# Optimization experiments

Measured on AMD Instinct MI355X. Metric: run time of the kernel, lower is better.

The kernel has to match this reference:

```python
import jax, jax.numpy as jnp
import numpy as np

# ---- static configuration (matches init_kwargs) ----
D_MODEL = 512
N_HEAD = 16
HEAD_DIM = D_MODEL // N_HEAD
SCALE = HEAD_DIM ** -0.5
SIZE = (64, 64)
WINDOW = (8, 8)
SHIFT = (4, 4)
WS = WINDOW[0] * WINDOW[1]          # tokens per window = 64
NW = (SIZE[0] // WINDOW[0]) * (SIZE[1] // WINDOW[1])  # windows per sample = 64


def _rel_pos_index(window):
    w0, w1 = window
    coords = np.stack(np.meshgrid(np.arange(w0), np.arange(w1), indexing='ij')).reshape(2, -1)
    rel = (coords[:, :, None] - coords[:, None, :]).transpose(1, 2, 0)  # [ws, ws, 2]
    rel[:, :, 0] += w0 - 1
    rel[:, :, 1] += w1 - 1
    rel[:, :, 0] *= 2 * w1 - 1
    return rel.sum(-1)  # [ws, ws] in [0, (2w0-1)(2w1-1))


def _shift_mask(size, window, shift):
    # Swin-style attention mask for shifted windows: 1.0 where tokens belong
    # to different cyclic-shift regions, else 0.0. Shape [nw, ws, ws].
    H, W = size
    w0, w1 = window
    s0, s1 = shift
    img = np.zeros((H, W))
    cnt = 0
    h_slices = (slice(0, -w0), slice(-w0, -s0), slice(-s0, None)) if s0 > 0 else (slice(None),)
    w_slices = (slice(0, -w1), slice(-w1, -s1), slice(-s1, None)) if s1 > 0 else (slice(None),)
    for hs in h_slices:
        for ws_ in w_slices:
            img[hs, ws_] = cnt
            cnt += 1
    win = img.reshape(H // w0, w0, W // w1, w1).transpose(0, 2, 1, 3).reshape(-1, w0 * w1)
    return (win[:, None, :] != win[:, :, None]).astype(np.float32)


REL_IDX = jnp.asarray(_rel_pos_index(WINDOW))              # [ws, ws] int
MASK = jnp.asarray(-100.0 * _shift_mask(SIZE, WINDOW, SHIFT))  # [nw, ws, ws]


def setup_inputs() -> dict:
    key = jax.random.key(0)
    k1, k2, k3, k4 = jax.random.split(key, 4)
    x = jax.random.normal(k1, (8, SIZE[0], SIZE[1], D_MODEL), dtype=jnp.float32)
    qkv_w = jax.random.normal(k2, (3 * D_MODEL, D_MODEL), dtype=jnp.float32) * (D_MODEL ** -0.5)
    qkv_b = jax.random.normal(k3, (3 * D_MODEL,), dtype=jnp.float32) * 0.02
    bias_table = jax.random.normal(k4, ((2 * WINDOW[0] - 1) * (2 * WINDOW[1] - 1), N_HEAD), dtype=jnp.float32) * 0.02
    return {"x": x, "qkv_w": qkv_w, "qkv_b": qkv_b, "bias_table": bias_table}


def reference(x, qkv_w, qkv_b, bias_table):
    n, H, W, c = x.shape
    w0, w1 = WINDOW
    # --- window partition: [n, H, W, c] -> [n*nw, ws, c] ---
    part = x.reshape(n, H // w0, w0, W // w1, w1, c)
    part = part.transpose(0, 1, 3, 2, 4, 5).reshape(n * NW, WS, c)
    # --- qkv projection ---
    qkv = (part @ qkv_w.T + qkv_b).reshape(n * NW, WS, 3, N_HEAD, HEAD_DIM)
    q, k, v = qkv[:, :, 0] * SCALE, qkv[:, :, 1], qkv[:, :, 2]
    # --- scores + relative bias + shift mask + softmax ---
    attn = jnp.einsum('wihd,wjhd->whij', q, k)  # [n*nw, nh, ws, ws]
    bias = bias_table[REL_IDX].transpose(2, 0, 1)  # [nh, ws, ws]
    attn = attn.reshape(n, NW, N_HEAD, WS, WS) + bias[None, None] + MASK[None, :, None]
    attn = jax.nn.softmax(attn, axis=-1).reshape(n * NW, N_HEAD, WS, WS)
    # --- AV + unpartition ---
    out = jnp.einsum('whij,wjhd->wihd', attn, v).reshape(n * NW, WS, c)
    out = out.reshape(n, H // w0, W // w1, w0, w1, c)
    return out.transpose(0, 1, 3, 2, 4, 5).reshape(n, H, W, c)
```

## Files before the change

kernel.cpp:

```cpp
#include <hip/hip_runtime.h>
#include <stdint.h>

typedef unsigned short u16;
typedef __attribute__((ext_vector_type(4))) float floatx4;
typedef __attribute__((ext_vector_type(8))) short bf16x8;

#define MTOK   32768
#define KDIM   512
#define NQKV   1536
#define NWIN   512
#define N_HEAD 16
#define SECSZ  (512 * 16 * 2048)
#define QK_SCALE 0.17677669529663687f

__device__ __forceinline__ u16 f2bf(float f) {
  union { float f; unsigned u; } v; v.f = f;
  unsigned r = v.u + 0x7fffu + ((v.u >> 16) & 1u);
  return (u16)(r >> 16);
}

__device__ __forceinline__ void load_lds16(const void* g, void* l) {
  __builtin_amdgcn_global_load_lds((const __attribute__((address_space(1))) void*)g,
                                   (__attribute__((address_space(3))) void*)l,
                                   16, 0, 0);
}

__global__ __launch_bounds__(256) void convert_xw(const float* __restrict__ x,
                                                  const float* __restrict__ wsrc,
                                                  const float* __restrict__ btab,
                                                  u16* __restrict__ A,
                                                  u16* __restrict__ Wb,
                                                  float* __restrict__ tbl) {
  int b = blockIdx.x;
  if (b < 768) {
    int e = (b * 256 + threadIdx.x) * 4;
    const float4 v = *(const float4*)(wsrc + e);
    ushort4 o;
    o.x = f2bf(v.x); o.y = f2bf(v.y); o.z = f2bf(v.z); o.w = f2bf(v.w);
    *(ushort4*)(Wb + e) = o;
  } else if (b < 17152) {
    int idx = (b - 768) * 256 + threadIdx.x;
    int e = idx * 4;
    int c = e & 511;
    int tg = e >> 9;
    int w = tg >> 6, t = tg & 63;
    int img = w >> 6, wy = (w >> 3) & 7, wx = w & 7;
    int ty = t >> 3, tx = t & 7;
    int y = wy * 8 + ty, xp = wx * 8 + tx;
    const float4 v = *(const float4*)(x + (((img * 64 + y) * 64 + xp) * 512 + c));
    ushort4 o;
    o.x = f2bf(v.x); o.y = f2bf(v.y); o.z = f2bf(v.z); o.w = f2bf(v.w);
    *(ushort4*)(A + e) = o;
  } else {
    int q = b - 17152;
    int cls = q >> 4, hh = q & 15;
    int ey = cls >> 1, ex = cls & 1;
    float* To = tbl + (q << 12);
#pragma unroll
    for (int e = 0; e < 16; ++e) {
      int idx = e * 256 + threadIdx.x;
      int i = idx >> 6, j = idx & 63;
      int ty = i >> 3, tx = i & 7, sy = j >> 3, sx = j & 7;
      int ry = ey ? (ty < 4 ? 1 : 2) : 0;
      int rx = ex ? (tx < 4 ? 1 : 2) : 0;
      int qy = ey ? (sy < 4 ? 1 : 2) : 0;
      int qx = ex ? (sx < 4 ? 1 : 2) : 0;
      float v = btab[((ty - sy + 7) * 15 + (tx - sx + 7)) * 16 + hh];
      if (ry * 3 + rx != qy * 3 + qx) v -= 100.0f;
      To[idx] = v;
    }
  }
}

__global__ __launch_bounds__(256, 4) void gemm_qkv(const u16* __restrict__ A,
                                                   const u16* __restrict__ Wb,
                                                   const float* __restrict__ bias,
                                                   u16* __restrict__ QKV) {
  __shared__ __attribute__((aligned(16))) char smem[32768];
  u16* Ct = (u16*)smem;

  int b = blockIdx.x;
  int xcd = b & 7, slot = b >> 3;
  int mtile = (slot / 12) * 8 + xcd;
  int ntile = slot % 12;

  int tid = threadIdx.x;
  int wv = tid >> 6, lane = tid & 63;
  int il = lane & 15, ch = lane >> 4;
  int wm = (wv & 1) * 64, wn = (wv >> 1) * 64;

  floatx4 acc[4][4];
  floatx4 zacc = {0.f, 0.f, 0.f, 0.f};
#pragma unroll
  for (int m = 0; m < 4; ++m)
#pragma unroll
    for (int n = 0; n < 4; ++n) acc[m][n] = zacc;

  int row0 = tid >> 2;
  int ch4 = (tid & 3) ^ (row0 & 3);
  const u16* Abase = A + (mtile * 128 + row0) * KDIM + ch4 * 8;
  const u16* Bbase = Wb + (ntile * 128 + row0) * KDIM + ch4 * 8;
  char* lAb = smem;
  char* lBb = smem + 16384;
  char* lA0s0 = lAb + wv * 1024;
  char* lA1s0 = lAb + 4096 + wv * 1024;
  char* lA0s1 = lAb + 8192 + wv * 1024;
  char* lA1s1 = lAb + 12288 + wv * 1024;
  char* lB0s0 = lBb + wv * 1024;
  char* lB1s0 = lBb + 4096 + wv * 1024;
  char* lB0s1 = lBb + 8192 + wv * 1024;
  char* lB1s1 = lBb + 12288 + wv * 1024;

  int sw = il & 3;
  for (int kb = 0; kb < KDIM; kb += 64) {
    __syncthreads();
    load_lds16(Abase + kb, lA0s0);
    load_lds16(Abase + kb + 64 * KDIM, lA1s0);
    load_lds16(Abase + kb + 32, lA0s1);
    load_lds16(Abase + kb + 32 + 64 * KDIM, lA1s1);
    load_lds16(Bbase + kb, lB0s0);
    load_lds16(Bbase + kb + 64 * KDIM, lB1s0);
    load_lds16(Bbase + kb + 32, lB0s1);
    load_lds16(Bbase + kb + 32 + 64 * KDIM, lB1s1);
    __syncthreads();

#pragma unroll
    for (int s = 0; s < 2; ++s) {
      const char* aB = lAb + s * 8192;
      const char* bB = lBb + s * 8192;
      bf16x8 af[4], bfr[4];
#pragma unroll
      for (int mt = 0; mt < 4; ++mt)
        af[mt] = *(const bf16x8*)(aB + (wm + mt * 16 + il) * 64 + (ch ^ sw) * 16);
#pragma unroll
      for (int nt = 0; nt < 4; ++nt)
        bfr[nt] = *(const bf16x8*)(bB + (wn + nt * 16 + il) * 64 + (ch ^ sw) * 16);
#pragma unroll
      for (int mt = 0; mt < 4; ++mt)
#pragma unroll
        for (int nt = 0; nt < 4; ++nt)
          acc[mt][nt] = __builtin_amdgcn_mfma_f32_16x16x32_bf16(af[mt], bfr[nt], acc[mt][nt], 0, 0, 0);
    }
  }

  __syncthreads();

  int sec = ntile >> 2;
  int h0 = (ntile & 3) * 4;
  int gw0 = mtile * 2;
  u16* dst = QKV + (size_t)sec * SECSZ;
  float sc = (sec == 0) ? QK_SCALE : 1.0f;

  for (int p = 0; p < 2; ++p) {
    if ((wv & 1) == p) {
      if (sec < 2) {
#pragma unroll
        for (int nt = 0; nt < 4; ++nt) {
          float bv = bias[ntile * 128 + wn + nt * 16 + il];
          int cl = wn + nt * 16 + il;
#pragma unroll
          for (int mt = 0; mt < 4; ++mt) {
            int lr = mt * 16 + ch * 4;
#pragma unroll
            for (int r = 0; r < 4; ++r)
              Ct[(lr + r) * 136 + cl] = f2bf((acc[mt][nt][r] + bv) * sc);
          }
        }
      } else {
#pragma unroll
        for (int nt = 0; nt < 4; ++nt) {
          float bv = bias[ntile * 128 + wn + nt * 16 + il];
          int cl = wn + nt * 16 + il;
#pragma unroll
          for (int mt = 0; mt < 4; ++mt) {
            int lr = mt * 16 + ch * 4;
            ushort4 pk;
            pk.x = f2bf(acc[mt][nt][0] + bv);
            pk.y = f2bf(acc[mt][nt][1] + bv);
            pk.z = f2bf(acc[mt][nt][2] + bv);
            pk.w = f2bf(acc[mt][nt][3] + bv);
            *(ushort4*)(Ct + cl * 72 + lr) = pk;
          }
        }
      }
    }
    __syncthreads();

    if (sec < 2) {
      int tl = tid >> 2, dc = tid & 3;
#pragma unroll
      for (int hl = 0; hl < 4; ++hl) {
        uint4 v = *(const uint4*)(smem + tl * 272 + hl * 64 + dc * 16);
        *(uint4*)(dst + ((gw0 + p) * 16 + h0 + hl) * 2048 + tl * 32 + dc * 8) = v;
      }
    } else {
      int c0 = tid >> 3, tq = tid & 7;
#pragma unroll
      for (int hl = 0; hl < 4; ++hl) {
        uint4 v = *(const uint4*)(smem + (hl * 32 + c0) * 144 + tq * 16);
        *(uint4*)(dst + ((gw0 + p) * 16 + h0 + hl) * 2048 + c0 * 64 + tq * 8) = v;
      }
    }
    __syncthreads();
  }
}

__global__ __launch_bounds__(256) void attn(const u16* __restrict__ QKV,
                                            const float* __restrict__ tbl,
                                            float* __restrict__ out) {
  __shared__ __attribute__((aligned(16))) u16 Pl[64 * 88];

  int bid = blockIdx.x;
  int w = bid >> 4, h = bid & 15;
  int tid = threadIdx.x;

  int lane = tid & 63, wv = tid >> 6;
  int il = lane & 15, ch = lane >> 4;
  const u16* Qb = QKV + (w * 16 + h) * 2048;
  const u16* Kb = Qb + SECSZ;
  const u16* Vt = Qb + 2 * (size_t)SECSZ;

  bf16x8 aq = *(const bf16x8*)(Qb + (wv * 16 + il) * 32 + ch * 8);
  floatx4 zacc = {0.f, 0.f, 0.f, 0.f};
  floatx4 s[4];
#pragma unroll
  for (int jt = 0; jt < 4; ++jt) {
    bf16x8 bk = *(const bf16x8*)(Kb + (jt * 16 + il) * 32 + ch * 8);
    s[jt] = __builtin_amdgcn_mfma_f32_16x16x32_bf16(aq, bk, zacc, 0, 0, 0);
  }

  bf16x8 bv0[2], bv1[2];
#pragma unroll
  for (int kk = 0; kk < 2; ++kk) {
    bv0[kk] = *(const bf16x8*)(Vt + il * 64 + kk * 32 + ch * 8);
    bv1[kk] = *(const bf16x8*)(Vt + (16 + il) * 64 + kk * 32 + ch * 8);
  }

  int winidx = w & 63;
  int wy = winidx >> 3, wx = winidx & 7;
  int cls = ((wy == 7) ? 2 : 0) | ((wx == 7) ? 1 : 0);
  const float* T = tbl + (((cls << 4) | h) << 12);

  float val[4][4];
#pragma unroll
  for (int r = 0; r < 4; ++r) {
    int i = wv * 16 + ch * 4 + r;
#pragma unroll
    for (int jt = 0; jt < 4; ++jt)
      val[r][jt] = s[jt][r] + T[i * 64 + jt * 16 + il];
  }

#pragma unroll
  for (int r = 0; r < 4; ++r) {
    float m = fmaxf(fmaxf(val[r][0], val[r][1]), fmaxf(val[r][2], val[r][3]));
    m = fmaxf(m, __shfl_xor(m, 1, 64));
    m = fmaxf(m, __shfl_xor(m, 2, 64));
    m = fmaxf(m, __shfl_xor(m, 4, 64));
    m = fmaxf(m, __shfl_xor(m, 8, 64));
    float sum = 0.f;
#pragma unroll
    for (int jt = 0; jt < 4; ++jt) { val[r][jt] = __expf(val[r][jt] - m); sum += val[r][jt]; }
    sum += __shfl_xor(sum, 1, 64);
    sum += __shfl_xor(sum, 2, 64);
    sum += __shfl_xor(sum, 4, 64);
    sum += __shfl_xor(sum, 8, 64);
    float inv = 1.0f / sum;
    int i = wv * 16 + ch * 4 + r;
#pragma unroll
    for (int jt = 0; jt < 4; ++jt)
      Pl[i * 88 + jt * 16 + il] = f2bf(val[r][jt] * inv);
  }

  asm volatile("s_waitcnt lgkmcnt(0)" ::: "memory");
  __builtin_amdgcn_sched_barrier(0);

  floatx4 o0 = zacc, o1 = zacc;
#pragma unroll
  for (int kk = 0; kk < 2; ++kk) {
    bf16x8 ap = *(const bf16x8*)((const u16*)Pl + (wv * 16 + il) * 88 + kk * 32 + ch * 8);
    o0 = __builtin_amdgcn_mfma_f32_16x16x32_bf16(ap, bv0[kk], o0, 0, 0, 0);
    o1 = __builtin_amdgcn_mfma_f32_16x16x32_bf16(ap, bv1[kk], o1, 0, 0, 0);
  }

  int img = w >> 6;
#pragma unroll
  for (int r = 0; r < 4; ++r) {
    int i = wv * 16 + ch * 4 + r;
    int ty = i >> 3, tx = i & 7;
    int y = wy * 8 + ty, xp = wx * 8 + tx;
    float* op = out + ((img * 64 + y) * 64 + xp) * 512 + h * 32;
    op[il] = o0[r];
    op[16 + il] = o1[r];
  }
}

extern "C" void kernel_launch(void* const* d_in, const int* in_sizes, int n_in,
                              void* d_out, int out_size, void* d_ws, size_t ws_size,
                              hipStream_t stream) {
  const float* x      = (const float*)d_in[0];
  const float* qkv_w  = (const float*)d_in[1];
  const float* qkv_b  = (const float*)d_in[2];
  const float* btab   = (const float*)d_in[3];
  float* out = (float*)d_out;

  char* ws = (char*)d_ws;
  u16* A    = (u16*)ws;
  u16* Wb   = (u16*)(ws + (size_t)MTOK * KDIM * 2);
  u16* QKV  = (u16*)(ws + (size_t)MTOK * KDIM * 2 + (size_t)NQKV * KDIM * 2);
  float* tbl = (float*)(ws + (size_t)MTOK * KDIM * 2 + (size_t)NQKV * KDIM * 2
                           + 3 * (size_t)SECSZ * 2);

  convert_xw<<<dim3(17216), dim3(256), 0, stream>>>(x, qkv_w, btab, A, Wb, tbl);
  gemm_qkv<<<dim3(3072), dim3(256), 0, stream>>>(A, Wb, qkv_b, QKV);
  attn<<<dim3(NWIN * N_HEAD), dim3(256), 0, stream>>>(QKV, tbl, out);
}
```

Before: 216.5 us.

## Double-buffer LDS tiles in QKV GEMM to overlap global loads with MFMA

Converts the QKV projection GEMM main loop from a single LDS buffer, with load-then-compute separated by barriers, to a two-stage ping-pong buffer. The next k-tile's global-to-LDS loads are issued before computing on the current one, with explicit vmcnt waits and barriers. This is meant to hide global memory latency behind MFMA work. It doubles LDS use to 64KB and lowers the launch-bounds occupancy hint from 4 to 2 blocks per CU, so fewer resident blocks are available for latency hiding.

```diff
diff --git a/kernel.cpp b/kernel.cpp
--- a/kernel.cpp
+++ b/kernel.cpp
@@ -72,11 +72,11 @@
   }
 }
 
-__global__ __launch_bounds__(256, 4) void gemm_qkv(const u16* __restrict__ A,
+__global__ __launch_bounds__(256, 2) void gemm_qkv(const u16* __restrict__ A,
                                                    const u16* __restrict__ Wb,
                                                    const float* __restrict__ bias,
                                                    u16* __restrict__ QKV) {
-  __shared__ __attribute__((aligned(16))) char smem[32768];
+  __shared__ __attribute__((aligned(16))) char smem[65536];
   u16* Ct = (u16*)smem;
 
   int b = blockIdx.x;
@@ -100,34 +100,38 @@
   int ch4 = (tid & 3) ^ (row0 & 3);
   const u16* Abase = A + (mtile * 128 + row0) * KDIM + ch4 * 8;
   const u16* Bbase = Wb + (ntile * 128 + row0) * KDIM + ch4 * 8;
-  char* lAb = smem;
-  char* lBb = smem + 16384;
-  char* lA0s0 = lAb + wv * 1024;
-  char* lA1s0 = lAb + 4096 + wv * 1024;
-  char* lA0s1 = lAb + 8192 + wv * 1024;
-  char* lA1s1 = lAb + 12288 + wv * 1024;
-  char* lB0s0 = lBb + wv * 1024;
-  char* lB1s0 = lBb + 4096 + wv * 1024;
-  char* lB0s1 = lBb + 8192 + wv * 1024;
-  char* lB1s1 = lBb + 12288 + wv * 1024;
+
+#define STAGE(d_, kb_)                                                  \
+  {                                                                     \
+    char* bb = smem + (d_) * 32768 + wv * 1024;                         \
+    load_lds16(Abase + (kb_), bb);                                      \
+    load_lds16(Abase + (kb_) + 64 * KDIM, bb + 4096);                   \
+    load_lds16(Abase + (kb_) + 32, bb + 8192);                          \
+    load_lds16(Abase + (kb_) + 32 + 64 * KDIM, bb + 12288);             \
+    load_lds16(Bbase + (kb_), bb + 16384);                              \
+    load_lds16(Bbase + (kb_) + 64 * KDIM, bb + 20480);                  \
+    load_lds16(Bbase + (kb_) + 32, bb + 24576);                         \
+    load_lds16(Bbase + (kb_) + 32 + 64 * KDIM, bb + 28672);             \
+  }
 
   int sw = il & 3;
-  for (int kb = 0; kb < KDIM; kb += 64) {
-    __syncthreads();
-    load_lds16(Abase + kb, lA0s0);
-    load_lds16(Abase + kb + 64 * KDIM, lA1s0);
-    load_lds16(Abase + kb + 32, lA0s1);
-    load_lds16(Abase + kb + 32 + 64 * KDIM, lA1s1);
-    load_lds16(Bbase + kb, lB0s0);
-    load_lds16(Bbase + kb + 64 * KDIM, lB1s0);
-    load_lds16(Bbase + kb + 32, lB0s1);
-    load_lds16(Bbase + kb + 32 + 64 * KDIM, lB1s1);
-    __syncthreads();
+  STAGE(0, 0);
+
+#pragma unroll
+  for (int t = 0; t < 8; ++t) {
+    const int cur = t & 1;
+    if (t < 7) {
+      STAGE(cur ^ 1, (t + 1) * 64);
+      asm volatile("s_waitcnt vmcnt(8)" ::: "memory");
+    } else {
+      asm volatile("s_waitcnt vmcnt(0)" ::: "memory");
+    }
+    __builtin_amdgcn_s_barrier();
 
 #pragma unroll
     for (int s = 0; s < 2; ++s) {
-      const char* aB = lAb + s * 8192;
-      const char* bB = lBb + s * 8192;
+      const char* aB = smem + cur * 32768 + s * 8192;
+      const char* bB = smem + cur * 32768 + 16384 + s * 8192;
       bf16x8 af[4], bfr[4];
 #pragma unroll
       for (int mt = 0; mt < 4; ++mt)
@@ -141,7 +145,11 @@
         for (int nt = 0; nt < 4; ++nt)
           acc[mt][nt] = __builtin_amdgcn_mfma_f32_16x16x32_bf16(af[mt], bfr[nt], acc[mt][nt], 0, 0, 0);
     }
-  }
+
+    asm volatile("s_waitcnt lgkmcnt(0)" ::: "memory");
+    __builtin_amdgcn_s_barrier();
+  }
+#undef STAGE
 
   __syncthreads();
 
```

New measurement: 223.9 us. 3.4% more time.
